# Performance work log

Hardware: AMD Instinct MI355X
Metric: run time of the kernel (lower is better)

## Reference

```python
import jax, jax.numpy as jnp
import numpy as np
from math import factorial

# ---- static config mirroring Cace.__init__ ----
MAX_L = 3            # max angular degree
N_RBF = 8            # Bessel radial basis size
RB = 8               # n_radial_basis (radial embedding dim after transform)
K = 3                # n_atom_basis -> edge channels C = K*K
NZ = 4               # len(zs)
CUTOFF = 5.5
N_NODES = 2000
N_EDGES = 50000
T_MP = 1             # num_message_passing
MP_NORM = 1.0 / np.sqrt(25.0)   # 1/sqrt(avg_num_neighbors)
C = K * K

def _lxlylz(max_l):
    out = []
    for l in range(max_l + 1):
        for lx in range(l, -1, -1):
            for ly in range(l - lx, -1, -1):
                out.append((lx, ly, l - lx - ly))
    return out

L_LIST = _lxlylz(MAX_L)                 # 20 Cartesian monomials for max_l=3
NL = len(L_LIST)
LX = np.array([t[0] for t in L_LIST]); LY = np.array([t[1] for t in L_LIST]); LZ = np.array([t[2] for t in L_LIST])
DEGS = LX + LY + LZ                     # degree l of each monomial
MULTI = np.array([factorial(int(d)) / (factorial(int(a)) * factorial(int(b)) * factorial(int(c)))
                  for a, b, c, d in zip(LX, LY, LZ, DEGS)], dtype=np.float32)
SEL = np.zeros((NL, MAX_L + 1), np.float32)
SEL[np.arange(NL), DEGS] = 1.0          # monomial -> degree one-hot (for per-l sums)
NB = 1 + (MAX_L + 1)                    # symmetrizer feats: nu=1 (l=0) + nu=2 per l

def bessel(r):  # [E] -> [E, N_RBF]
    n = jnp.arange(1, N_RBF + 1, dtype=r.dtype)
    return jnp.sqrt(2.0 / CUTOFF) * jnp.sin(n[None, :] * jnp.pi * r[:, None] / CUTOFF) / r[:, None]

def poly_cutoff(r):  # MACE-style polynomial cutoff, p=6
    p = 6.0
    u = r / CUTOFF
    f = 1.0 - (p + 1.0) * (p + 2.0) / 2.0 * u**6 + p * (p + 2.0) * u**7 - p * (p + 1.0) / 2.0 * u**8
    return f * (u < 1.0)

def axis_pows(x):  # [E] -> [E, MAX_L+1] = x^0..x^MAX_L (safe grads, handles negatives)
    pows = [jnp.ones_like(x)]
    for _ in range(MAX_L):
        pows.append(pows[-1] * x)
    return jnp.stack(pows, axis=1)

def angular(u):  # unit vectors [E,3] -> Cartesian monomials [E, NL]
    return axis_pows(u[:, 0])[:, LX] * axis_pows(u[:, 1])[:, LY] * axis_pows(u[:, 2])[:, LZ]

def radial_transform(x, W):  # x [N,R,L,C], W [MAX_L+1,R,Rb] shared per degree l
    return jnp.einsum('nrlc,lrb->nblc', x, W[DEGS])

def symmetrize(A):  # A [N,Rb,NL,C] -> B [N,Rb,NB,C]
    b1 = A[:, :, :1, :]  # nu=1: the (0,0,0) monomial (index 0)
    w = (A * A) * jnp.asarray(MULTI)[None, None, :, None]
    b2 = jnp.einsum('nrlc,lm->nrmc', w, jnp.asarray(SEL))  # nu=2 invariant per degree l
    return jnp.concatenate([b1, b2], axis=2)


def setup_inputs() -> dict:
    key = jax.random.key(0)
    ks = jax.random.split(key, 9)
    positions = jax.random.uniform(ks[0], (N_NODES, 3), dtype=jnp.float32) * 12.0
    species = jax.random.randint(ks[1], (N_NODES,), 0, NZ)
    send = jax.random.randint(ks[2], (N_EDGES,), 0, N_NODES)
    off = jax.random.randint(ks[3], (N_EDGES,), 1, N_NODES)
    recv = (send + off) % N_NODES  # no self-edges -> strictly positive edge lengths
    edge_index = jnp.stack([send, recv])
    shifts = jnp.zeros((N_EDGES, 3), jnp.float32)
    W_embed = jax.random.normal(ks[4], (NZ, K), jnp.float32)
    W_radial = jax.random.normal(ks[5], (MAX_L + 1, N_RBF, RB), jnp.float32) / np.sqrt(N_RBF)
    W_mem = jax.random.normal(ks[6], (MAX_L + 1, RB, RB), jnp.float32) / np.sqrt(RB)
    W_ar = jax.random.normal(ks[7], (N_RBF, RB), jnp.float32) / np.sqrt(N_RBF)
    W_chi = jax.random.normal(ks[8], (RB, NB), jnp.float32) * 0.1
    return {"positions": positions, "shifts": shifts, "W_embed": W_embed, "W_radial": W_radial,
            "W_mem": W_mem, "W_ar": W_ar, "W_chi": W_chi, "species": species, "edge_index": edge_index}


def reference(positions, shifts, W_embed, W_radial, W_mem, W_ar, W_chi, species, edge_index):
    n_nodes = positions.shape[0]
    send, recv = edge_index[0], edge_index[1]
    # edge geometry
    vec = positions[recv] - positions[send] + shifts
    lengths = jnp.linalg.norm(vec, axis=-1)
    u = vec / (lengths[:, None] + 1e-9)
    rad = bessel(lengths)          # [E,R]
    fcut = poly_cutoff(lengths)    # [E]
    ang = angular(u)               # [E,NL]
    # edge type encoding: outer product of sender/receiver species embeddings
    emb = W_embed[species]         # [N,K]
    enc = (emb[send][:, :, None] * emb[recv][:, None, :]).reshape(-1, C)  # [E,C]
    # elementwise_multiply_3tensors -> [E,R,NL,C]
    edge_attri = jnp.einsum('er,el,ec->erlc', rad * fcut[:, None], ang, enc)
    A = radial_transform(jax.ops.segment_sum(edge_attri, recv, num_segments=n_nodes), W_radial)  # [N,Rb,NL,C]
    B = symmetrize(A)              # [N,Rb,NB,C]
    feats = [B]
    for _ in range(T_MP):
        mem = jnp.einsum('nrlc,lrb->nblc', A, W_mem[DEGS])        # NodeMemory
        chi = jnp.einsum('nbkc,bk->nc', B, W_chi)                  # MessageBchi node scalar
        msg_bchi = edge_attri * chi[send][:, None, None, :]
        A_bchi = radial_transform(jax.ops.segment_sum(msg_bchi, recv, num_segments=n_nodes), W_radial)
        fr = (rad @ W_ar) * fcut[:, None]                          # MessageAr radial filter [E,Rb]
        msg_ar = A[send] * fr[:, :, None, None]
        A_ar = jax.ops.segment_sum(msg_ar, recv, num_segments=n_nodes)
        A = (A_ar + A_bchi) * MP_NORM + mem
        B = symmetrize(A)
        feats.append(B)
    return jnp.stack(feats, axis=-1)   # [N,Rb,NB,C,T_MP+1]
```

## Files before the change

### kernel.cpp

```cpp
#include <hip/hip_runtime.h>
#include <hip/hip_bf16.h>


#define CUTF 5.5f
#define MPNORM 0.2f

__constant__ int   d_DEGS[20]  = {0,1,1,1,2,2,2,2,2,2,3,3,3,3,3,3,3,3,3,3};
__constant__ float d_MULTI[20] = {1,1,1,1,1,2,2,1,2,1,1,3,3,3,6,3,1,3,3,1};

__global__ void k_edge(const float* __restrict__ pos,
                       const float* __restrict__ shifts,
                       const float* __restrict__ Wemb,
                       const float* __restrict__ War,
                       const int* __restrict__ species,
                       const int* __restrict__ eidx,
                       float* __restrict__ edata,
                       int* __restrict__ counts,
                       int E) {
  __shared__ float war_s[64];
  int t = threadIdx.x;
  if (t < 64) war_s[t] = War[t];
  __syncthreads();
  int e = blockIdx.x * blockDim.x + t;
  if (e >= E) return;
  int s  = eidx[e];
  int rI = eidx[E + e];
  float vx = pos[rI*3+0] - pos[s*3+0] + shifts[e*3+0];
  float vy = pos[rI*3+1] - pos[s*3+1] + shifts[e*3+1];
  float vz = pos[rI*3+2] - pos[s*3+2] + shifts[e*3+2];
  float len = sqrtf(vx*vx + vy*vy + vz*vz);
  float inv = 1.0f / (len + 1e-9f);
  float ux = vx*inv, uy = vy*inv, uz = vz*inv;
  float uu = len * (1.0f/CUTF);
  float u2 = uu*uu, u6 = u2*u2*u2;
  float fcut = (uu < 1.0f) ? (1.0f - 28.0f*u6 + 48.0f*u6*uu - 21.0f*u6*u2) : 0.0f;
  float x = 3.14159265358979f * uu;
  float sn = sinf(x), c2 = 2.0f*cosf(x), snm1 = 0.0f;
  float pref = sqrtf(2.0f/CUTF) / (len + 1e-20f);
  float rad[8], g[8];
  #pragma unroll
  for (int k = 0; k < 8; k++) {
    rad[k] = pref * sn;
    g[k]   = rad[k] * fcut;
    float nxt = c2*sn - snm1; snm1 = sn; sn = nxt;
  }
  float* eb = edata + (size_t)e * 64;
  #pragma unroll
  for (int k = 0; k < 8; k++) eb[k] = g[k];
  #pragma unroll
  for (int b = 0; b < 8; b++) {
    float a = 0.0f;
    #pragma unroll
    for (int k = 0; k < 8; k++) a += rad[k] * war_s[k*8+b];
    eb[8+b] = a * fcut;
  }
  float px2 = ux*ux, py2 = uy*uy, pz2 = uz*uz;
  eb[16] = 1.0f; eb[17] = ux;     eb[18] = uy;     eb[19] = uz;
  eb[20] = px2;  eb[21] = ux*uy;  eb[22] = ux*uz;  eb[23] = py2;
  eb[24] = uy*uz;eb[25] = pz2;
  eb[26] = px2*ux; eb[27] = px2*uy; eb[28] = px2*uz; eb[29] = ux*py2;
  eb[30] = ux*uy*uz; eb[31] = ux*pz2; eb[32] = py2*uy; eb[33] = py2*uz;
  eb[34] = uy*pz2; eb[35] = pz2*uz;
  int zs = species[s], zr = species[rI];
  float es0 = Wemb[zs*3+0], es1 = Wemb[zs*3+1], es2 = Wemb[zs*3+2];
  float er0 = Wemb[zr*3+0], er1 = Wemb[zr*3+1], er2 = Wemb[zr*3+2];
  eb[36] = es0*er0; eb[37] = es0*er1; eb[38] = es0*er2;
  eb[39] = es1*er0; eb[40] = es1*er1; eb[41] = es1*er2;
  eb[42] = es2*er0; eb[43] = es2*er1; eb[44] = es2*er2;
  atomicAdd(&counts[rI], 1);
}

__global__ void k_scan(const int* __restrict__ counts, int* __restrict__ offs, int N) {
  __shared__ int part[256];
  int t = threadIdx.x;
  int local[8]; int sum = 0;
  #pragma unroll
  for (int i = 0; i < 8; i++) {
    int idx = t*8 + i;
    int v = (idx < N) ? counts[idx] : 0;
    local[i] = sum; sum += v;
  }
  part[t] = sum; __syncthreads();
  for (int d = 1; d < 256; d <<= 1) {
    int add = (t >= d) ? part[t-d] : 0;
    __syncthreads();
    part[t] += add;
    __syncthreads();
  }
  int excl = part[t] - sum;
  #pragma unroll
  for (int i = 0; i < 8; i++) {
    int idx = t*8 + i;
    if (idx < N) offs[idx] = excl + local[i];
  }
  if (t == 255) offs[N] = part[255];
}

__global__ void k_fill(const int* __restrict__ eidx, const int* __restrict__ offs,
                       int* __restrict__ cursor, int* __restrict__ order, int E) {
  int e = blockIdx.x * blockDim.x + threadIdx.x;
  if (e >= E) return;
  int rI = eidx[E + e];
  int slot = atomicAdd(&cursor[rI], 1);
  order[offs[rI] + slot] = e;
}

__global__ __launch_bounds__(192) void k_nodeA(
    const float* __restrict__ edata, const int* __restrict__ order,
    const int* __restrict__ offs,
    const float* __restrict__ Wrad, const float* __restrict__ Wchi,
    float* __restrict__ A, unsigned int* __restrict__ Abf2,
    float* __restrict__ chi, float* __restrict__ out, int N) {
  __shared__ float wr_s[288];
  __shared__ float wchi_s[40];
  __shared__ float Bsh[360];
  int t = threadIdx.x, n = blockIdx.x;
  for (int i = t; i < 256; i += 192) { int d = i >> 6, rm = i & 63; wr_s[d*72+rm] = Wrad[i]; }
  for (int i = t; i < 40;  i += 192) wchi_s[i] = Wchi[i];
  for (int i = t; i < 360; i += 192) Bsh[i] = 0.0f;
  int l = t / 9, c = t - l*9;
  bool act = t < 180;
  int ll = act ? l : 0, cc = act ? c : 0;
  float acc[8];
  #pragma unroll
  for (int r = 0; r < 8; r++) acc[r] = 0.0f;
  int start = offs[n], end = offs[n+1];
  #pragma unroll 4
  for (int j = start; j < end; j++) {
    int e = order[j];
    const float* row = edata + (size_t)e * 64;
    float p = row[16+ll] * row[36+cc];
    #pragma unroll
    for (int r = 0; r < 8; r++) acc[r] += row[r] * p;
  }
  __syncthreads();
  int deg = act ? d_DEGS[l] : 0;
  const float* wp = &wr_s[deg*72];
  float Ab[8];
  #pragma unroll
  for (int b = 0; b < 8; b++) {
    float a = 0.0f;
    #pragma unroll
    for (int r = 0; r < 8; r++) a += acc[r] * wp[r*8+b];
    Ab[b] = a;
  }
  if (act) {
    #pragma unroll
    for (int b = 0; b < 8; b++) A[(size_t)n*1440 + t*8 + b] = Ab[b];
    #pragma unroll
    for (int bp = 0; bp < 4; bp++) {
      __hip_bfloat16 blo = __float2bfloat16(Ab[2*bp]);
      __hip_bfloat16 bhi = __float2bfloat16(Ab[2*bp+1]);
      unsigned int pr = (unsigned int)(*reinterpret_cast<unsigned short*>(&blo))
                      | ((unsigned int)(*reinterpret_cast<unsigned short*>(&bhi)) << 16);
      Abf2[(size_t)bp*N*180 + (size_t)n*180 + t] = pr;
    }
    if (l == 0) {
      #pragma unroll
      for (int b = 0; b < 8; b++) Bsh[b*45 + c] = Ab[b];
    }
    float m = d_MULTI[l]; int k = 1 + deg;
    #pragma unroll
    for (int b = 0; b < 8; b++) atomicAdd(&Bsh[b*45 + k*9 + c], m*Ab[b]*Ab[b]);
  }
  __syncthreads();
  if (t < 9) {
    float s = 0.0f;
    for (int b = 0; b < 8; b++)
      #pragma unroll
      for (int k = 0; k < 5; k++) s += Bsh[b*45 + k*9 + t] * wchi_s[b*5 + k];
    chi[n*9 + t] = s;
  }
  for (int i = t; i < 360; i += 192)
    out[((size_t)n*360 + i)*2 + 0] = Bsh[i];
}

__global__ __launch_bounds__(192) void k_node2(
    const float* __restrict__ edata, const int* __restrict__ order,
    const int* __restrict__ offs, const int* __restrict__ eidx,
    const float* __restrict__ Wrad, const float* __restrict__ Wmem,
    const float* __restrict__ A, const unsigned int* __restrict__ Abf2,
    const float* __restrict__ chi, float* __restrict__ out, int N) {
  __shared__ float wr_s[288], wm_s[288];
  __shared__ float Bsh[360];
  int t = threadIdx.x, n = blockIdx.x;
  for (int i = t; i < 256; i += 192) {
    int d = i >> 6, rm = i & 63;
    wr_s[d*72+rm] = Wrad[i];
    wm_s[d*72+rm] = Wmem[i];
  }
  for (int i = t; i < 360; i += 192) Bsh[i] = 0.0f;
  int l = t / 9, c = t - l*9;
  bool act = t < 180;
  int ll = act ? l : 0, cc = act ? c : 0;
  int tt = act ? t : 0;
  size_t plane = (size_t)N * 180;
  float Sacc[8], ARacc[8];
  #pragma unroll
  for (int r = 0; r < 8; r++) { Sacc[r] = 0.0f; ARacc[r] = 0.0f; }
  int start = offs[n], end = offs[n+1];
  #pragma unroll 4
  for (int j = start; j < end; j++) {
    int e = order[j];
    const float* row = edata + (size_t)e * 64;
    int snd = eidx[e];
    float ch = chi[snd*9 + cc];
    float pch = row[16+ll] * row[36+cc] * ch;
    #pragma unroll
    for (int r = 0; r < 8; r++) Sacc[r] += row[r] * pch;
    const unsigned int* gp = Abf2 + (size_t)snd*180 + tt;
    unsigned int q0 = gp[0];
    unsigned int q1 = gp[plane];
    unsigned int q2 = gp[2*plane];
    unsigned int q3 = gp[3*plane];
    float a0 = __uint_as_float(q0 << 16), a1 = __uint_as_float(q0 & 0xffff0000u);
    float a2 = __uint_as_float(q1 << 16), a3 = __uint_as_float(q1 & 0xffff0000u);
    float a4 = __uint_as_float(q2 << 16), a5 = __uint_as_float(q2 & 0xffff0000u);
    float a6 = __uint_as_float(q3 << 16), a7 = __uint_as_float(q3 & 0xffff0000u);
    ARacc[0] += a0*row[8];  ARacc[1] += a1*row[9];
    ARacc[2] += a2*row[10]; ARacc[3] += a3*row[11];
    ARacc[4] += a4*row[12]; ARacc[5] += a5*row[13];
    ARacc[6] += a6*row[14]; ARacc[7] += a7*row[15];
  }
  __syncthreads();
  float newA[8];
  if (act) {
    int deg = d_DEGS[l];
    const float* wrp = &wr_s[deg*72];
    const float* wmp = &wm_s[deg*72];
    const float* aop = A + (size_t)n*1440 + t*8;
    float aown[8];
    #pragma unroll
    for (int r = 0; r < 8; r++) aown[r] = aop[r];
    #pragma unroll
    for (int b = 0; b < 8; b++) {
      float mem = 0.0f, ab = 0.0f;
      #pragma unroll
      for (int r = 0; r < 8; r++) { mem += aown[r]*wmp[r*8+b]; ab += Sacc[r]*wrp[r*8+b]; }
      newA[b] = (ARacc[b] + ab)*MPNORM + mem;
    }
    if (l == 0) {
      #pragma unroll
      for (int b = 0; b < 8; b++) Bsh[b*45 + c] = newA[b];
    }
    float m = d_MULTI[l]; int k = 1 + d_DEGS[l];
    #pragma unroll
    for (int b = 0; b < 8; b++) atomicAdd(&Bsh[b*45 + k*9 + c], m*newA[b]*newA[b]);
  }
  __syncthreads();
  for (int i = t; i < 360; i += 192)
    out[((size_t)n*360 + i)*2 + 1] = Bsh[i];
}

extern "C" void kernel_launch(void* const* d_in, const int* in_sizes, int n_in,
                              void* d_out, int out_size, void* d_ws, size_t ws_size,
                              hipStream_t stream) {
  const float* pos    = (const float*)d_in[0];
  const float* shifts = (const float*)d_in[1];
  const float* Wemb   = (const float*)d_in[2];
  const float* Wrad   = (const float*)d_in[3];
  const float* Wmem   = (const float*)d_in[4];
  const float* War    = (const float*)d_in[5];
  const float* Wchi   = (const float*)d_in[6];
  const int* species = (const int*)d_in[7];
  const int* eidx    = (const int*)d_in[8];
  float* out = (float*)d_out;
  int N = in_sizes[7];
  int E = in_sizes[8] / 2;

  char* base = (char*)d_ws;
  size_t off = 0;
  float* edata = (float*)(base + off); off += (size_t)E*64*4;
  float* A     = (float*)(base + off); off += (size_t)N*1440*4;
  unsigned int* Abf2 = (unsigned int*)(base + off); off += (size_t)N*180*4*4;
  float* chi   = (float*)(base + off); off += (size_t)N*9*4;
  int* counts  = (int*)(base + off);   off += (size_t)N*4;
  int* cursor  = (int*)(base + off);   off += (size_t)N*4;
  int* offs    = (int*)(base + off);   off += (((size_t)(N+1)*4) + 15) & ~(size_t)15;
  int* order   = (int*)(base + off);   off += (size_t)E*4;

  hipMemsetAsync(counts, 0, (size_t)N*2*4, stream);
  int eb = (E + 255) / 256;
  k_edge<<<eb, 256, 0, stream>>>(pos, shifts, Wemb, War, species, eidx, edata, counts, E);
  k_scan<<<1, 256, 0, stream>>>(counts, offs, N);
  k_fill<<<eb, 256, 0, stream>>>(eidx, offs, cursor, order, E);
  k_nodeA<<<N, 192, 0, stream>>>(edata, order, offs, Wrad, Wchi, A, Abf2, chi, out, N);
  k_node2<<<N, 192, 0, stream>>>(edata, order, offs, eidx, Wrad, Wmem, A, Abf2, chi, out, N);
}
```

Measured before the change: 172.6 us.

## Process several nodes per block, vectorize edge stores, write interleaved output once

Each node block now handles four nodes in sequence, so the shared-memory weight loads are amortised over more work. The edge kernel builds its row in registers and writes it as float4 vectors instead of scalar stores. The first-layer B features go to a workspace buffer, and the second kernel writes both timesteps as float2 pairs, replacing the strided 2-way interleaved scalar writes. The cost is fewer blocks (500 on a large GPU), which lowers parallelism and latency hiding.

```diff
diff --git a/kernel.cpp b/kernel.cpp
--- a/kernel.cpp
+++ b/kernel.cpp
@@ -4,6 +4,7 @@
 
 #define CUTF 5.5f
 #define MPNORM 0.2f
+#define NPB 4
 
 __constant__ int   d_DEGS[20]  = {0,1,1,1,2,2,2,2,2,2,3,3,3,3,3,3,3,3,3,3};
 __constant__ float d_MULTI[20] = {1,1,1,1,1,2,2,1,2,1,1,3,3,3,6,3,1,3,3,1};
@@ -37,36 +38,39 @@
   float x = 3.14159265358979f * uu;
   float sn = sinf(x), c2 = 2.0f*cosf(x), snm1 = 0.0f;
   float pref = sqrtf(2.0f/CUTF) / (len + 1e-20f);
-  float rad[8], g[8];
+  float rad[8];
+  float v[48];
   #pragma unroll
   for (int k = 0; k < 8; k++) {
     rad[k] = pref * sn;
-    g[k]   = rad[k] * fcut;
+    v[k]   = rad[k] * fcut;
     float nxt = c2*sn - snm1; snm1 = sn; sn = nxt;
   }
-  float* eb = edata + (size_t)e * 64;
-  #pragma unroll
-  for (int k = 0; k < 8; k++) eb[k] = g[k];
   #pragma unroll
   for (int b = 0; b < 8; b++) {
     float a = 0.0f;
     #pragma unroll
     for (int k = 0; k < 8; k++) a += rad[k] * war_s[k*8+b];
-    eb[8+b] = a * fcut;
+    v[8+b] = a * fcut;
   }
   float px2 = ux*ux, py2 = uy*uy, pz2 = uz*uz;
-  eb[16] = 1.0f; eb[17] = ux;     eb[18] = uy;     eb[19] = uz;
-  eb[20] = px2;  eb[21] = ux*uy;  eb[22] = ux*uz;  eb[23] = py2;
-  eb[24] = uy*uz;eb[25] = pz2;
-  eb[26] = px2*ux; eb[27] = px2*uy; eb[28] = px2*uz; eb[29] = ux*py2;
-  eb[30] = ux*uy*uz; eb[31] = ux*pz2; eb[32] = py2*uy; eb[33] = py2*uz;
-  eb[34] = uy*pz2; eb[35] = pz2*uz;
+  v[16] = 1.0f; v[17] = ux;     v[18] = uy;     v[19] = uz;
+  v[20] = px2;  v[21] = ux*uy;  v[22] = ux*uz;  v[23] = py2;
+  v[24] = uy*uz;v[25] = pz2;
+  v[26] = px2*ux; v[27] = px2*uy; v[28] = px2*uz; v[29] = ux*py2;
+  v[30] = ux*uy*uz; v[31] = ux*pz2; v[32] = py2*uy; v[33] = py2*uz;
+  v[34] = uy*pz2; v[35] = pz2*uz;
   int zs = species[s], zr = species[rI];
   float es0 = Wemb[zs*3+0], es1 = Wemb[zs*3+1], es2 = Wemb[zs*3+2];
   float er0 = Wemb[zr*3+0], er1 = Wemb[zr*3+1], er2 = Wemb[zr*3+2];
-  eb[36] = es0*er0; eb[37] = es0*er1; eb[38] = es0*er2;
-  eb[39] = es1*er0; eb[40] = es1*er1; eb[41] = es1*er2;
-  eb[42] = es2*er0; eb[43] = es2*er1; eb[44] = es2*er2;
+  v[36] = es0*er0; v[37] = es0*er1; v[38] = es0*er2;
+  v[39] = es1*er0; v[40] = es1*er1; v[41] = es1*er2;
+  v[42] = es2*er0; v[43] = es2*er1; v[44] = es2*er2;
+  v[45] = 0.0f; v[46] = 0.0f; v[47] = 0.0f;
+  float4* eb4 = reinterpret_cast<float4*>(edata + (size_t)e * 64);
+  #pragma unroll
+  for (int w = 0; w < 12; w++)
+    eb4[w] = make_float4(v[4*w], v[4*w+1], v[4*w+2], v[4*w+3]);
   atomicAdd(&counts[rI], 1);
 }
 
@@ -110,69 +114,76 @@
     const int* __restrict__ offs,
     const float* __restrict__ Wrad, const float* __restrict__ Wchi,
     float* __restrict__ A, unsigned int* __restrict__ Abf2,
-    float* __restrict__ chi, float* __restrict__ out, int N) {
+    float* __restrict__ chi, float* __restrict__ B0, int N) {
   __shared__ float wr_s[288];
   __shared__ float wchi_s[40];
   __shared__ float Bsh[360];
-  int t = threadIdx.x, n = blockIdx.x;
+  int t = threadIdx.x;
   for (int i = t; i < 256; i += 192) { int d = i >> 6, rm = i & 63; wr_s[d*72+rm] = Wrad[i]; }
   for (int i = t; i < 40;  i += 192) wchi_s[i] = Wchi[i];
-  for (int i = t; i < 360; i += 192) Bsh[i] = 0.0f;
   int l = t / 9, c = t - l*9;
   bool act = t < 180;
   int ll = act ? l : 0, cc = act ? c : 0;
-  float acc[8];
-  #pragma unroll
-  for (int r = 0; r < 8; r++) acc[r] = 0.0f;
-  int start = offs[n], end = offs[n+1];
-  #pragma unroll 4
-  for (int j = start; j < end; j++) {
-    int e = order[j];
-    const float* row = edata + (size_t)e * 64;
-    float p = row[16+ll] * row[36+cc];
+  int deg = act ? d_DEGS[ll] : 0;
+  float mlt = act ? d_MULTI[ll] : 0.0f;
+  const float* wp = &wr_s[deg*72];
+
+  for (int k0 = 0; k0 < NPB; k0++) {
+    int n = blockIdx.x * NPB + k0;
+    if (n >= N) break;
+    __syncthreads();
+    for (int i = t; i < 360; i += 192) Bsh[i] = 0.0f;
+    float acc[8];
     #pragma unroll
-    for (int r = 0; r < 8; r++) acc[r] += row[r] * p;
-  }
-  __syncthreads();
-  int deg = act ? d_DEGS[l] : 0;
-  const float* wp = &wr_s[deg*72];
-  float Ab[8];
-  #pragma unroll
-  for (int b = 0; b < 8; b++) {
-    float a = 0.0f;
+    for (int r = 0; r < 8; r++) acc[r] = 0.0f;
+    int start = offs[n], end = offs[n+1];
+    #pragma unroll 4
+    for (int j = start; j < end; j++) {
+      int e = order[j];
+      const float* row = edata + (size_t)e * 64;
+      float p = row[16+ll] * row[36+cc];
+      #pragma unroll
+      for (int r = 0; r < 8; r++) acc[r] += row[r] * p;
+    }
+    __syncthreads();
+    float Ab[8];
     #pragma unroll
-    for (int r = 0; r < 8; r++) a += acc[r] * wp[r*8+b];
-    Ab[b] = a;
-  }
-  if (act) {
-    #pragma unroll
-    for (int b = 0; b < 8; b++) A[(size_t)n*1440 + t*8 + b] = Ab[b];
-    #pragma unroll
-    for (int bp = 0; bp < 4; bp++) {
-      __hip_bfloat16 blo = __float2bfloat16(Ab[2*bp]);
-      __hip_bfloat16 bhi = __float2bfloat16(Ab[2*bp+1]);
-      unsigned int pr = (unsigned int)(*reinterpret_cast<unsigned short*>(&blo))
-                      | ((unsigned int)(*reinterpret_cast<unsigned short*>(&bhi)) << 16);
-      Abf2[(size_t)bp*N*180 + (size_t)n*180 + t] = pr;
-    }
-    if (l == 0) {
-      #pragma unroll
-      for (int b = 0; b < 8; b++) Bsh[b*45 + c] = Ab[b];
-    }
-    float m = d_MULTI[l]; int k = 1 + deg;
-    #pragma unroll
-    for (int b = 0; b < 8; b++) atomicAdd(&Bsh[b*45 + k*9 + c], m*Ab[b]*Ab[b]);
-  }
-  __syncthreads();
-  if (t < 9) {
-    float s = 0.0f;
-    for (int b = 0; b < 8; b++)
-      #pragma unroll
-      for (int k = 0; k < 5; k++) s += Bsh[b*45 + k*9 + t] * wchi_s[b*5 + k];
-    chi[n*9 + t] = s;
-  }
-  for (int i = t; i < 360; i += 192)
-    out[((size_t)n*360 + i)*2 + 0] = Bsh[i];
+    for (int b = 0; b < 8; b++) {
+      float a = 0.0f;
+      #pragma unroll
+      for (int r = 0; r < 8; r++) a += acc[r] * wp[r*8+b];
+      Ab[b] = a;
+    }
+    if (act) {
+      #pragma unroll
+      for (int b = 0; b < 8; b++) A[(size_t)n*1440 + t*8 + b] = Ab[b];
+      #pragma unroll
+      for (int bp = 0; bp < 4; bp++) {
+        __hip_bfloat16 blo = __float2bfloat16(Ab[2*bp]);
+        __hip_bfloat16 bhi = __float2bfloat16(Ab[2*bp+1]);
+        unsigned int pr = (unsigned int)(*reinterpret_cast<unsigned short*>(&blo))
+                        | ((unsigned int)(*reinterpret_cast<unsigned short*>(&bhi)) << 16);
+        Abf2[(size_t)bp*N*180 + (size_t)n*180 + t] = pr;
+      }
+      if (l == 0) {
+        #pragma unroll
+        for (int b = 0; b < 8; b++) Bsh[b*45 + c] = Ab[b];
+      }
+      int kk = 1 + deg;
+      #pragma unroll
+      for (int b = 0; b < 8; b++) atomicAdd(&Bsh[b*45 + kk*9 + c], mlt*Ab[b]*Ab[b]);
+    }
+    __syncthreads();
+    if (t < 9) {
+      float s = 0.0f;
+      for (int b = 0; b < 8; b++)
+        #pragma unroll
+        for (int kq = 0; kq < 5; kq++) s += Bsh[b*45 + kq*9 + t] * wchi_s[b*5 + kq];
+      chi[n*9 + t] = s;
+    }
+    for (int i = t; i < 360; i += 192)
+      B0[(size_t)n*360 + i] = Bsh[i];
+  }
 }
 
 __global__ __launch_bounds__(192) void k_node2(
@@ -180,76 +191,87 @@
     const int* __restrict__ offs, const int* __restrict__ eidx,
     const float* __restrict__ Wrad, const float* __restrict__ Wmem,
     const float* __restrict__ A, const unsigned int* __restrict__ Abf2,
-    const float* __restrict__ chi, float* __restrict__ out, int N) {
+    const float* __restrict__ chi, const float* __restrict__ B0,
+    float* __restrict__ out, int N) {
   __shared__ float wr_s[288], wm_s[288];
   __shared__ float Bsh[360];
-  int t = threadIdx.x, n = blockIdx.x;
+  int t = threadIdx.x;
   for (int i = t; i < 256; i += 192) {
     int d = i >> 6, rm = i & 63;
     wr_s[d*72+rm] = Wrad[i];
     wm_s[d*72+rm] = Wmem[i];
   }
-  for (int i = t; i < 360; i += 192) Bsh[i] = 0.0f;
   int l = t / 9, c = t - l*9;
   bool act = t < 180;
   int ll = act ? l : 0, cc = act ? c : 0;
   int tt = act ? t : 0;
+  int deg = act ? d_DEGS[ll] : 0;
+  float mlt = act ? d_MULTI[ll] : 0.0f;
+  const float* wrp = &wr_s[deg*72];
+  const float* wmp = &wm_s[deg*72];
   size_t plane = (size_t)N * 180;
-  float Sacc[8], ARacc[8];
-  #pragma unroll
-  for (int r = 0; r < 8; r++) { Sacc[r] = 0.0f; ARacc[r] = 0.0f; }
-  int start = offs[n], end = offs[n+1];
-  #pragma unroll 4
-  for (int j = start; j < end; j++) {
-    int e = order[j];
-    const float* row = edata + (size_t)e * 64;
-    int snd = eidx[e];
-    float ch = chi[snd*9 + cc];
-    float pch = row[16+ll] * row[36+cc] * ch;
+
+  for (int k0 = 0; k0 < NPB; k0++) {
+    int n = blockIdx.x * NPB + k0;
+    if (n >= N) break;
+    __syncthreads();
+    for (int i = t; i < 360; i += 192) Bsh[i] = 0.0f;
+    float Sacc[8], ARacc[8];
     #pragma unroll
-    for (int r = 0; r < 8; r++) Sacc[r] += row[r] * pch;
-    const unsigned int* gp = Abf2 + (size_t)snd*180 + tt;
-    unsigned int q0 = gp[0];
-    unsigned int q1 = gp[plane];
-    unsigned int q2 = gp[2*plane];
-    unsigned int q3 = gp[3*plane];
-    float a0 = __uint_as_float(q0 << 16), a1 = __uint_as_float(q0 & 0xffff0000u);
-    float a2 = __uint_as_float(q1 << 16), a3 = __uint_as_float(q1 & 0xffff0000u);
-    float a4 = __uint_as_float(q2 << 16), a5 = __uint_as_float(q2 & 0xffff0000u);
-    float a6 = __uint_as_float(q3 << 16), a7 = __uint_as_float(q3 & 0xffff0000u);
-    ARacc[0] += a0*row[8];  ARacc[1] += a1*row[9];
-    ARacc[2] += a2*row[10]; ARacc[3] += a3*row[11];
-    ARacc[4] += a4*row[12]; ARacc[5] += a5*row[13];
-    ARacc[6] += a6*row[14]; ARacc[7] += a7*row[15];
-  }
-  __syncthreads();
-  float newA[8];
-  if (act) {
-    int deg = d_DEGS[l];
-    const float* wrp = &wr_s[deg*72];
-    const float* wmp = &wm_s[deg*72];
-    const float* aop = A + (size_t)n*1440 + t*8;
-    float aown[8];
-    #pragma unroll
-    for (int r = 0; r < 8; r++) aown[r] = aop[r];
-    #pragma unroll
-    for (int b = 0; b < 8; b++) {
-      float mem = 0.0f, ab = 0.0f;
-      #pragma unroll
-      for (int r = 0; r < 8; r++) { mem += aown[r]*wmp[r*8+b]; ab += Sacc[r]*wrp[r*8+b]; }
-      newA[b] = (ARacc[b] + ab)*MPNORM + mem;
-    }
-    if (l == 0) {
-      #pragma unroll
-      for (int b = 0; b < 8; b++) Bsh[b*45 + c] = newA[b];
-    }
-    float m = d_MULTI[l]; int k = 1 + d_DEGS[l];
-    #pragma unroll
-    for (int b = 0; b < 8; b++) atomicAdd(&Bsh[b*45 + k*9 + c], m*newA[b]*newA[b]);
-  }
-  __syncthreads();
-  for (int i = t; i < 360; i += 192)
-    out[((size_t)n*360 + i)*2 + 1] = Bsh[i];
+    for (int r = 0; r < 8; r++) { Sacc[r] = 0.0f; ARacc[r] = 0.0f; }
+    int start = offs[n], end = offs[n+1];
+    #pragma unroll 4
+    for (int j = start; j < end; j++) {
+      int e = order[j];
+      const float* row = edata + (size_t)e * 64;
+      int snd = eidx[e];
+      float ch = chi[snd*9 + cc];
+      float pch = row[16+ll] * row[36+cc] * ch;
+      #pragma unroll
+      for (int r = 0; r < 8; r++) Sacc[r] += row[r] * pch;
+      const unsigned int* gp = Abf2 + (size_t)snd*180 + tt;
+      unsigned int q0 = gp[0];
+      unsigned int q1 = gp[plane];
+      unsigned int q2 = gp[2*plane];
+      unsigned int q3 = gp[3*plane];
+      float a0 = __uint_as_float(q0 << 16), a1 = __uint_as_float(q0 & 0xffff0000u);
+      float a2 = __uint_as_float(q1 << 16), a3 = __uint_as_float(q1 & 0xffff0000u);
+      float a4 = __uint_as_float(q2 << 16), a5 = __uint_as_float(q2 & 0xffff0000u);
+      float a6 = __uint_as_float(q3 << 16), a7 = __uint_as_float(q3 & 0xffff0000u);
+      ARacc[0] += a0*row[8];  ARacc[1] += a1*row[9];
+      ARacc[2] += a2*row[10]; ARacc[3] += a3*row[11];
+      ARacc[4] += a4*row[12]; ARacc[5] += a5*row[13];
+      ARacc[6] += a6*row[14]; ARacc[7] += a7*row[15];
+    }
+    __syncthreads();
+    if (act) {
+      const float* aop = A + (size_t)n*1440 + t*8;
+      float aown[8];
+      #pragma unroll
+      for (int r = 0; r < 8; r++) aown[r] = aop[r];
+      float newA[8];
+      #pragma unroll
+      for (int b = 0; b < 8; b++) {
+        float mem = 0.0f, ab = 0.0f;
+        #pragma unroll
+        for (int r = 0; r < 8; r++) { mem += aown[r]*wmp[r*8+b]; ab += Sacc[r]*wrp[r*8+b]; }
+        newA[b] = (ARacc[b] + ab)*MPNORM + mem;
+      }
+      if (l == 0) {
+        #pragma unroll
+        for (int b = 0; b < 8; b++) Bsh[b*45 + c] = newA[b];
+      }
+      int kk = 1 + deg;
+      #pragma unroll
+      for (int b = 0; b < 8; b++) atomicAdd(&Bsh[b*45 + kk*9 + c], mlt*newA[b]*newA[b]);
+    }
+    __syncthreads();
+    float2* out2 = reinterpret_cast<float2*>(out);
+    for (int i = t; i < 360; i += 192) {
+      float2 pk; pk.x = B0[(size_t)n*360 + i]; pk.y = Bsh[i];
+      out2[(size_t)n*360 + i] = pk;
+    }
+  }
 }
 
 extern "C" void kernel_launch(void* const* d_in, const int* in_sizes, int n_in,
@@ -274,6 +296,7 @@
   float* A     = (float*)(base + off); off += (size_t)N*1440*4;
   unsigned int* Abf2 = (unsigned int*)(base + off); off += (size_t)N*180*4*4;
   float* chi   = (float*)(base + off); off += (size_t)N*9*4;
+  float* B0    = (float*)(base + off); off += (size_t)N*360*4;
   int* counts  = (int*)(base + off);   off += (size_t)N*4;
   int* cursor  = (int*)(base + off);   off += (size_t)N*4;
   int* offs    = (int*)(base + off);   off += (((size_t)(N+1)*4) + 15) & ~(size_t)15;
@@ -281,9 +304,10 @@
 
   hipMemsetAsync(counts, 0, (size_t)N*2*4, stream);
   int eb = (E + 255) / 256;
+  int nb = (N + NPB - 1) / NPB;
   k_edge<<<eb, 256, 0, stream>>>(pos, shifts, Wemb, War, species, eidx, edata, counts, E);
   k_scan<<<1, 256, 0, stream>>>(counts, offs, N);
   k_fill<<<eb, 256, 0, stream>>>(eidx, offs, cursor, order, E);
-  k_nodeA<<<N, 192, 0, stream>>>(edata, order, offs, Wrad, Wchi, A, Abf2, chi, out, N);
-  k_node2<<<N, 192, 0, stream>>>(edata, order, offs, eidx, Wrad, Wmem, A, Abf2, chi, out, N);
-}
+  k_nodeA<<<nb, 192, 0, stream>>>(edata, order, offs, Wrad, Wchi, A, Abf2, chi, B0, N);
+  k_node2<<<nb, 192, 0, stream>>>(edata, order, offs, eidx, Wrad, Wmem, A, Abf2, chi, B0, out, N);
+}
```

After: 203.1 us. 17.7% more time.
